# Optimization experiments

Measured on AMD Instinct MI355X. Metric: run time of the kernel, lower is better.

## Reference

```python
import jax, jax.numpy as jnp
import numpy as np

L = 50
N_INIT = 3.5      # initial radius n
N_STEP = 0.5      # n_step
NUM_ADJ_PARM = 0.1
NUM_CANDS = 256   # candidate radii n + k*n_step


def _leaky(x):
    return jax.nn.leaky_relu(x, negative_slope=0.01)


def _conv(x, w, b):
    y = jax.lax.conv_general_dilated(x, w, (1, 1), 'VALID',
                                     dimension_numbers=('NCHW', 'OIHW', 'NCHW'))
    return y + b[None, :, None, None]


def _maxpool2(x):
    return jax.lax.reduce_window(x, -jnp.inf, jax.lax.max,
                                 (1, 1, 2, 2), (1, 1, 2, 2), 'VALID')


def _sage(x, adj, w_rel, b_rel, w_root):
    # PyG DenseSAGEConv: lin_rel(mean-agg) + lin_root(x), normalize=False
    agg = adj @ x
    deg = jnp.clip(jnp.sum(adj, axis=-1, keepdims=True), 1.0, None)
    return (agg / deg) @ w_rel.T + b_rel + x @ w_root.T


def _build_adj(h):
    # fused pairwise euclidean distance + radius threshold with retry:
    # smallest radius in {n + k*n_step} whose (directed) edge count >= 0.1*N
    g = h @ h.T                                   # [N,N] gram
    sq = jnp.diag(g)
    dist = jnp.sqrt(jnp.maximum(sq[:, None] - 2.0 * g + sq[None, :], 0.0))
    n = h.shape[0]
    eye = jnp.eye(n, dtype=bool)
    d_sorted = jnp.sort(jnp.where(eye, jnp.inf, dist).reshape(-1))
    cands = N_INIT + N_STEP * jnp.arange(NUM_CANDS, dtype=dist.dtype)
    counts = jnp.searchsorted(d_sorted, cands)    # edges with dist < cand
    thr = cands[jnp.argmax(counts >= NUM_ADJ_PARM * n)]
    A = ((dist < thr) & (~eye)).astype(h.dtype)
    return jax.lax.stop_gradient(A)               # edge list is non-diff in torch too


def _diff_pool(z, a, s):
    # PyG dense_diff_pool (link + entropy losses; only link loss l1 is returned)
    s = jax.nn.softmax(s, axis=-1)
    x = s.T @ z
    adj = s.T @ a @ s
    l1 = jnp.linalg.norm(a - s @ s.T) / (a.shape[0] * a.shape[1])
    return x, adj, l1


def setup_inputs() -> dict:
    key = jax.random.key(0)
    ks = jax.random.split(key, 19)
    def w(k, shape, scale=0.05):
        return scale * jax.random.normal(k, shape, dtype=jnp.float32)
    N = 4096  # bag size / number of graph nodes
    return {
        'x': jax.random.normal(ks[0], (1, N, 1, 28, 28), dtype=jnp.float32),
        'conv1_w': w(ks[1], (20, 1, 5, 5)),
        'conv1_b': w(ks[2], (20,)),
        'conv2_w': w(ks[3], (50, 20, 5, 5)),
        'conv2_b': w(ks[4], (50,)),
        'fc_w': w(ks[5], (50, 800)),
        'fc_b': w(ks[6], (50,)),
        'embd_rel_w': w(ks[7], (50, 50)),
        'embd_rel_b': w(ks[8], (50,)),
        'embd_root_w': w(ks[9], (50, 50)),
        'pool_rel_w': w(ks[10], (1, 50)),
        'pool_rel_b': w(ks[11], (1,)),
        'pool_root_w': w(ks[12], (1, 50)),
        'mlp_w': w(ks[13], (1, 1)),
        'mlp_b': w(ks[14], (1,)),
        'lin1_w': w(ks[15], (25, 50)),
        'lin1_b': w(ks[16], (25,)),
        'lin2_w': w(ks[17], (2, 25)),
        'lin2_b': w(ks[18], (2,)),
    }


def reference(x, conv1_w, conv1_b, conv2_w, conv2_b, fc_w, fc_b,
              embd_rel_w, embd_rel_b, embd_root_w,
              pool_rel_w, pool_rel_b, pool_root_w,
              mlp_w, mlp_b, lin1_w, lin1_b, lin2_w, lin2_b):
    xi = x[0]                                             # squeeze(0): [N,1,28,28]
    h = _maxpool2(jax.nn.relu(_conv(xi, conv1_w, conv1_b)))   # [N,20,12,12]
    h = _maxpool2(jax.nn.relu(_conv(h, conv2_w, conv2_b)))    # [N,50,4,4]
    h = h.reshape(h.shape[0], -1)                         # [N,800]
    h = jax.nn.relu(h @ fc_w.T + fc_b)                    # [N,50]
    A = _build_adj(h)                                     # [N,N] dense adjacency
    Z = _leaky(_sage(h, A, embd_rel_w, embd_rel_b, embd_root_w))   # [N,50]
    S = _leaky(_sage(h, A, pool_rel_w, pool_rel_b, pool_root_w))   # [N,1]
    S = _leaky(S @ mlp_w.T + mlp_b)                       # [N,1]
    Xp, adjp, l1 = _diff_pool(Z, A, S)                    # [1,50], [1,1]
    Xp = _leaky(_sage(Xp, adjp, embd_rel_w, embd_rel_b, embd_root_w))  # reuses gnn_embd
    v = Xp.reshape(-1)                                    # [50]
    v = _leaky(v @ lin1_w.T + lin1_b)                     # [25]
    v = _leaky(v @ lin2_w.T + lin2_b)                     # [2]
    p = jax.nn.softmax(v, axis=0)
    return jnp.max(p), jnp.argmax(p), l1
```

## Files before the change

### kernel.cpp

```cpp
#include <hip/hip_runtime.h>
#include <hip/hip_bf16.h>

#define AGG_OFF     0u
#define DEG_OFF     819200u
#define XP_OFF      835584u
#define HIST_OFF    835840u
#define SCAL_OFF    836992u
#define S_OFF       837120u
#define H_OFF       1048576u
#define HT_OFF      1867776u
#define SQ_OFF      2686976u
#define BYTES_OFF   2703360u
#define WS_NEED     (2703360ull + 16777216ull)

__global__ __launch_bounds__(256) void mil_init(unsigned int* __restrict__ w)
{
    w[(size_t)blockIdx.x * 256u + threadIdx.x] = 0u;
}

__global__ __launch_bounds__(256, 2) void mil_cnn(
    const float* __restrict__ x, const float* __restrict__ w1, const float* __restrict__ b1,
    const float* __restrict__ w2, const float* __restrict__ b2,
    const float* __restrict__ fcw, const float* __restrict__ fcb,
    float* __restrict__ hout, float* __restrict__ hT, float* __restrict__ sqout)
{
    __shared__ __align__(16) float pool1[20*144];
    __shared__ __align__(16) float pool2[800];
    __shared__ float b1s[20];
    __shared__ float b2s[64];
    __shared__ float hloc[64];
    __shared__ __align__(16) float ovl[3200];

    float* img = ovl;
    float* w1s = ovl + 784;
    float* w2s = ovl;

    const int n = blockIdx.x;
    const int t = threadIdx.x;

    const float* xin = x + (size_t)n * 784;
    for (int i = t; i < 784; i += 256) img[i] = xin[i];
    for (int i = t; i < 500; i += 256) w1s[i] = w1[i];
    if (t < 20) b1s[t] = b1[t];
    { int u = t - 32; if (u >= 0 && u < 50) b2s[u] = b2[u]; }
    __syncthreads();

    if (t < 240) {
        const int c = t / 12, py = t % 12;
        float wr[25];
#pragma unroll
        for (int k = 0; k < 25; k++) wr[k] = w1s[c*25 + k];
        float acc0[24], acc1[24];
#pragma unroll
        for (int i = 0; i < 24; i++) { acc0[i] = 0.f; acc1[i] = 0.f; }
#pragma unroll
        for (int j = 0; j < 6; j++) {
            float rr[28];
            const float* rp = &img[(2*py + j)*28];
#pragma unroll
            for (int q = 0; q < 7; q++) {
                const float4 v = *(const float4*)(rp + 4*q);
                rr[4*q+0] = v.x; rr[4*q+1] = v.y; rr[4*q+2] = v.z; rr[4*q+3] = v.w;
            }
            if (j <= 4) {
#pragma unroll
                for (int kx = 0; kx < 5; kx++) {
                    const float wv = wr[j*5 + kx];
#pragma unroll
                    for (int xo = 0; xo < 24; xo++)
                        acc0[xo] = fmaf(rr[xo+kx], wv, acc0[xo]);
                }
            }
            if (j >= 1) {
#pragma unroll
                for (int kx = 0; kx < 5; kx++) {
                    const float wv = wr[(j-1)*5 + kx];
#pragma unroll
                    for (int xo = 0; xo < 24; xo++)
                        acc1[xo] = fmaf(rr[xo+kx], wv, acc1[xo]);
                }
            }
        }
        const float bias = b1s[c];
#pragma unroll
        for (int px = 0; px < 12; px++) {
            float v = fmaxf(fmaxf(acc0[2*px], acc0[2*px+1]),
                            fmaxf(acc1[2*px], acc1[2*px+1]));
            pool1[c*144 + py*12 + px] = fmaxf(v + bias, 0.f);
        }
    }
    __syncthreads();

    float acc2[16];
#pragma unroll
    for (int i = 0; i < 16; i++) acc2[i] = 0.f;
    const int c2 = t >> 2, py2 = t & 3;
    const int rswz = (c2 & 7) << 2;
    for (int cig = 0; cig < 10; cig++) {
        __syncthreads();
        for (int idx = t; idx < 3200; idx += 256) {
            const int cc = idx >> 6, cl = (idx >> 5) & 1, k = idx & 31;
            const float v = (k < 25) ? w2[cc*500 + (cig*2 + cl)*25 + k] : 0.f;
            w2s[(idx & ~31) | (k ^ ((cc & 7) << 2))] = v;
        }
        __syncthreads();
        if (t < 200) {
#pragma unroll
            for (int cl = 0; cl < 2; cl++) {
                const int ci = cig*2 + cl;
                float wreg[25];
                const int wbase = c2*64 + cl*32;
#pragma unroll
                for (int g = 0; g < 6; g++) {
                    const float4 v = *(const float4*)&w2s[wbase + (4*g ^ rswz)];
                    wreg[4*g+0] = v.x; wreg[4*g+1] = v.y;
                    wreg[4*g+2] = v.z; wreg[4*g+3] = v.w;
                }
                wreg[24] = w2s[wbase + (24 ^ rswz)];
#pragma unroll
                for (int j = 0; j < 6; j++) {
                    float rr[12];
                    const float* rp = &pool1[ci*144 + (2*py2 + j)*12];
#pragma unroll
                    for (int q = 0; q < 3; q++) {
                        const float4 v = *(const float4*)(rp + 4*q);
                        rr[4*q+0] = v.x; rr[4*q+1] = v.y;
                        rr[4*q+2] = v.z; rr[4*q+3] = v.w;
                    }
                    if (j <= 4) {
#pragma unroll
                        for (int kx = 0; kx < 5; kx++) {
                            const float wv = wreg[j*5 + kx];
#pragma unroll
                            for (int xo = 0; xo < 8; xo++)
                                acc2[xo] = fmaf(rr[xo+kx], wv, acc2[xo]);
                        }
                    }
                    if (j >= 1) {
#pragma unroll
                        for (int kx = 0; kx < 5; kx++) {
                            const float wv = wreg[(j-1)*5 + kx];
#pragma unroll
                            for (int xo = 0; xo < 8; xo++)
                                acc2[8+xo] = fmaf(rr[xo+kx], wv, acc2[8+xo]);
                        }
                    }
                }
            }
        }
    }
    __syncthreads();
    if (t < 200) {
        const float bias = b2s[c2];
#pragma unroll
        for (int px = 0; px < 4; px++) {
            float v = fmaxf(fmaxf(acc2[2*px], acc2[2*px+1]),
                            fmaxf(acc2[8+2*px], acc2[8+2*px+1]));
            pool2[c2*16 + py2*4 + px] = fmaxf(v + bias, 0.f);
        }
    }
    __syncthreads();

    {
        const int wv = t >> 6, lane = t & 63;
        for (int o = wv; o < 50; o += 4) {
            float acc = 0.f;
#pragma unroll
            for (int r = 0; r < 13; r++) {
                const int k = r*64 + lane;
                if (k < 800) acc = fmaf(fcw[o*800 + k], pool2[k], acc);
            }
#pragma unroll
            for (int off = 32; off > 0; off >>= 1) acc += __shfl_xor(acc, off);
            if (lane == 0) hloc[o] = fmaxf(acc + fcb[o], 0.f);
        }
    }
    __syncthreads();
    if (t < 50) {
        const float v = hloc[t];
        hout[(size_t)n*50 + t] = v;
        hT[(size_t)t*4096 + n] = v;
    }
    if (t < 64) {
        float s = (t < 50) ? hloc[t]*hloc[t] : 0.f;
#pragma unroll
        for (int off = 32; off > 0; off >>= 1) s += __shfl_xor(s, off);
        if (t == 0) sqout[n] = s;
    }
}

__global__ __launch_bounds__(256) void mil_colsum(
    const float* __restrict__ hT, float* __restrict__ S)
{
    __shared__ float red[4];
    const int d = blockIdx.x, t = threadIdx.x;
    float s = 0.f;
    for (int nn = t; nn < 4096; nn += 256) s += hT[(size_t)d*4096 + nn];
#pragma unroll
    for (int off = 32; off > 0; off >>= 1) s += __shfl_xor(s, off);
    if ((t & 63) == 0) red[t >> 6] = s;
    __syncthreads();
    if (t == 0) S[d] = red[0] + red[1] + red[2] + red[3];
}

__global__ __launch_bounds__(256, 3) void mil_hist(
    const float* __restrict__ hT, const float* __restrict__ sq,
    unsigned int* __restrict__ hist, unsigned char* __restrict__ bytesA,
    const int wb)
{
    __shared__ __align__(16) float hiT[6400];
    __shared__ __align__(16) float hjT[6400];
    __shared__ float sqi[128], sqj[128];
    __shared__ unsigned int lh[257];

    const int t = threadIdx.x;
    const int i0 = blockIdx.x * 128, j0 = blockIdx.y * 128;

    for (int idx = t; idx < 6400; idx += 256) {
        const int c = idx >> 7, l = idx & 127;
        hiT[idx] = hT[(size_t)c*4096 + i0 + l];
        hjT[idx] = hT[(size_t)c*4096 + j0 + l];
    }
    if (t < 128) { sqi[t] = sq[i0 + t]; sqj[t] = sq[j0 + t]; }
    for (int idx = t; idx < 257; idx += 256) lh[idx] = 0;
    __syncthreads();

    const int ti = t >> 4, tj = t & 15;
    float acc[8][8];
#pragma unroll
    for (int a = 0; a < 8; a++)
#pragma unroll
        for (int b = 0; b < 8; b++) acc[a][b] = 0.f;

    for (int c = 0; c < 50; c++) {
        const float4 a0 = *(const float4*)&hiT[c*128 + ti*8];
        const float4 a1 = *(const float4*)&hiT[c*128 + ti*8 + 4];
        const float4 b0 = *(const float4*)&hjT[c*128 + tj*8];
        const float4 b1 = *(const float4*)&hjT[c*128 + tj*8 + 4];
        const float aa[8] = {a0.x,a0.y,a0.z,a0.w,a1.x,a1.y,a1.z,a1.w};
        const float bb[8] = {b0.x,b0.y,b0.z,b0.w,b1.x,b1.y,b1.z,b1.w};
#pragma unroll
        for (int a = 0; a < 8; a++)
#pragma unroll
            for (int b = 0; b < 8; b++)
                acc[a][b] = fmaf(aa[a], bb[b], acc[a][b]);
    }

    unsigned int cnt0 = 0;
#pragma unroll
    for (int a = 0; a < 8; a++) {
        unsigned pk0 = 0, pk1 = 0;
#pragma unroll
        for (int b = 0; b < 8; b++) {
            const int gi = i0 + ti*8 + a, gj = j0 + tj*8 + b;
            int kbyte = 255;
            if (gi != gj) {
                const float d2 = sqi[ti*8+a] + sqj[tj*8+b] - 2.f*acc[a][b];
                const float d = sqrtf(fmaxf(d2, 0.f));
                int k = (int)floorf((d - 3.5f)*2.f) + 1;
                k = k < 0 ? 0 : (k > 256 ? 256 : k);
                if (k > 0   && d <  3.5f + 0.5f*(float)(k-1)) k--;
                if (k < 256 && d >= 3.5f + 0.5f*(float)k)     k++;
                if (k == 0) cnt0++;
                else atomicAdd(&lh[k], 1u);
                kbyte = k < 255 ? k : 255;
            }
            if (b < 4) pk0 |= (unsigned)kbyte << (8*b);
            else       pk1 |= (unsigned)kbyte << (8*(b-4));
        }
        if (wb) {
            const int gi = i0 + ti*8 + a;
            *(uint2*)&bytesA[(size_t)gi*4096 + j0 + tj*8] = make_uint2(pk0, pk1);
        }
    }
#pragma unroll
    for (int off = 32; off > 0; off >>= 1) cnt0 += __shfl_xor(cnt0, off);
    if ((t & 63) == 0 && cnt0) atomicAdd(&lh[0], cnt0);
    __syncthreads();
    for (int idx = t; idx < 257; idx += 256)
        if (lh[idx]) atomicAdd(&hist[idx], lh[idx]);
}

__global__ void mil_scan(const unsigned int* __restrict__ hist, int* __restrict__ scal)
{
    if (threadIdx.x == 0) {
        unsigned long long cum = 0, nz = 0;
        int kc = -1;
        for (int k = 0; k < 256; k++) {
            cum += hist[k];
            if (kc < 0 && cum >= 410ull) { kc = k; nz = cum; }
        }
        if (kc < 0) { kc = 0; nz = hist[0]; }
        scal[0] = kc;
        scal[1] = (int)nz;
        scal[2] = (nz * 2ull > 16773120ull) ? 1 : 0;
        scal[3] = (kc >= 255) ? 1 : 0;
    }
}

__global__ __launch_bounds__(256) void mil_agg_b(
    const float* __restrict__ h, const unsigned char* __restrict__ bytesA,
    const int* __restrict__ scal, float* __restrict__ agg, float* __restrict__ deg)
{
    __shared__ __align__(16) unsigned char bL[64*528];
    __shared__ __align__(16) float hsub[4096];
    if (scal[3] != 0) return;
    const int t = threadIdx.x;
    const int i0 = blockIdx.x * 64;
    const int jg = blockIdx.y * 512;
    const int kc = scal[0];
    const bool inv = (scal[2] != 0);

    for (int idx = t; idx < 2048; idx += 256) {
        const int r = idx >> 5, c = idx & 31;
        *(uint4*)&bL[r*528 + c*16] =
            *(const uint4*)&bytesA[(size_t)(i0 + r)*4096 + jg + c*16];
    }

    const int il = t >> 2, dq = t & 3;
    const int gi = i0 + il;
    float accum[16];
#pragma unroll
    for (int i = 0; i < 16; i++) accum[i] = 0.f;
    int degc = 0;

    for (int js = 0; js < 8; js++) {
        __syncthreads();
        for (int idx = t; idx < 4096; idx += 256) {
            const int jj = idx >> 6, d = idx & 63;
            hsub[idx] = (d < 50) ? h[(size_t)(jg + js*64 + jj)*50 + d] : 0.f;
        }
        __syncthreads();
        const unsigned char* brow = &bL[il*528 + js*64];
        const int jbase = jg + js*64;
        for (int jj = 0; jj < 64; jj++) {
            const bool e = (jbase + jj != gi) && ((brow[jj] <= kc) != inv);
            if (!__any(e)) continue;
            const float m = e ? 1.f : 0.f;
            if (e && dq == 0) degc++;
#pragma unroll
            for (int q = 0; q < 4; q++) {
                const float4 hv = *(const float4*)&hsub[jj*64 + dq*16 + q*4];
                accum[q*4+0] = fmaf(m, hv.x, accum[q*4+0]);
                accum[q*4+1] = fmaf(m, hv.y, accum[q*4+1]);
                accum[q*4+2] = fmaf(m, hv.z, accum[q*4+2]);
                accum[q*4+3] = fmaf(m, hv.w, accum[q*4+3]);
            }
        }
    }

#pragma unroll
    for (int q = 0; q < 4; q++)
#pragma unroll
        for (int rr = 0; rr < 4; rr++) {
            const int d = dq*16 + q*4 + rr;
            if (d < 50 && accum[q*4+rr] != 0.f)
                atomicAdd(&agg[(size_t)gi*50 + d], accum[q*4+rr]);
        }
    if (dq == 0 && degc) atomicAdd(&deg[gi], (float)degc);
}

__global__ __launch_bounds__(256, 3) void mil_agg_r(
    const float* __restrict__ h, const float* __restrict__ hT, const float* __restrict__ sq,
    const int* __restrict__ scal, float* __restrict__ agg, float* __restrict__ deg,
    const int mode)
{
    __shared__ __align__(16) float hiT[3200];
    __shared__ __align__(16) float hjT[3200];
    __shared__ float sqi[64], sqj[64];
    __shared__ __align__(16) float hsub[4096];
    __shared__ __align__(16) unsigned char mk[4096];

    if (mode == 1 && scal[3] == 0) return;
    const int t = threadIdx.x;
    const int i0 = blockIdx.x * 64;
    const float thr = 3.5f + 0.5f * (float)scal[0];
    const bool inv = (scal[2] != 0);

    for (int idx = t; idx < 3200; idx += 256) {
        const int c = idx >> 6, l = idx & 63;
        hiT[idx] = hT[(size_t)c*4096 + i0 + l];
    }
    if (t < 64) sqi[t] = sq[i0 + t];

    const int ti = t >> 4, tj = t & 15;
    const int il = t >> 2, dq = t & 3;
    float accum[16];
#pragma unroll
    for (int i = 0; i < 16; i++) accum[i] = 0.f;
    int degc = 0;

    for (int js = 0; js < 8; js++) {
        const int j0 = blockIdx.y * 512 + js * 64;
        __syncthreads();
        for (int idx = t; idx < 3200; idx += 256) {
            const int c = idx >> 6, l = idx & 63;
            hjT[idx] = hT[(size_t)c*4096 + j0 + l];
        }
        for (int idx = t; idx < 4096; idx += 256) {
            const int jj = idx >> 6, d = idx & 63;
            hsub[idx] = (d < 50) ? h[(size_t)(j0 + jj)*50 + d] : 0.f;
        }
        if (t < 64) sqj[t] = sq[j0 + t];
        __syncthreads();

        float acc[4][4];
#pragma unroll
        for (int a = 0; a < 4; a++)
#pragma unroll
            for (int b = 0; b < 4; b++) acc[a][b] = 0.f;
        for (int c = 0; c < 50; c++) {
            const float4 av = *(const float4*)&hiT[c*64 + ti*4];
            const float4 bv = *(const float4*)&hjT[c*64 + tj*4];
            const float aa[4] = {av.x, av.y, av.z, av.w};
            const float bb[4] = {bv.x, bv.y, bv.z, bv.w};
#pragma unroll
            for (int a = 0; a < 4; a++)
#pragma unroll
                for (int b = 0; b < 4; b++)
                    acc[a][b] = fmaf(aa[a], bb[b], acc[a][b]);
        }

#pragma unroll
        for (int b = 0; b < 4; b++) {
            unsigned char ob[4];
#pragma unroll
            for (int a = 0; a < 4; a++) {
                const int gi = i0 + ti*4 + a, gj = j0 + tj*4 + b;
                const float d2 = sqi[ti*4+a] + sqj[tj*4+b] - 2.f*acc[a][b];
                const float dd = sqrtf(fmaxf(d2, 0.f));
                const bool edge = (dd < thr);
                ob[a] = (gi != gj && (edge != inv)) ? 1 : 0;
            }
            *(uchar4*)&mk[(tj*4+b)*64 + ti*4] = make_uchar4(ob[0], ob[1], ob[2], ob[3]);
        }
        __syncthreads();

        for (int jj = 0; jj < 64; jj++) {
            const bool e = (mk[jj*64 + il] != 0);
            if (!__any(e)) continue;
            const float m = e ? 1.f : 0.f;
            if (e && dq == 0) degc++;
#pragma unroll
            for (int q = 0; q < 4; q++) {
                const float4 hv = *(const float4*)&hsub[jj*64 + dq*16 + q*4];
                accum[q*4+0] = fmaf(m, hv.x, accum[q*4+0]);
                accum[q*4+1] = fmaf(m, hv.y, accum[q*4+1]);
                accum[q*4+2] = fmaf(m, hv.z, accum[q*4+2]);
                accum[q*4+3] = fmaf(m, hv.w, accum[q*4+3]);
            }
        }
    }

    const int node = i0 + il;
#pragma unroll
    for (int q = 0; q < 4; q++)
#pragma unroll
        for (int rr = 0; rr < 4; rr++) {
            const int d = dq*16 + q*4 + rr;
            if (d < 50 && accum[q*4+rr] != 0.f)
                atomicAdd(&agg[(size_t)node*50 + d], accum[q*4+rr]);
        }
    if (dq == 0 && degc) atomicAdd(&deg[node], (float)degc);
}

__global__ __launch_bounds__(256) void mil_sage(
    const float* __restrict__ h, const float* __restrict__ agg, const float* __restrict__ deg,
    const float* __restrict__ S, const int* __restrict__ scal,
    const float* __restrict__ relw, const float* __restrict__ relb,
    const float* __restrict__ rootw, float* __restrict__ Xp)
{
    __shared__ float relT[2500];
    __shared__ float rootT[2500];
    __shared__ float rb[50];
    __shared__ float hn[250], mn[250], zb[250];
    const int t = threadIdx.x;
    const int nb = blockIdx.x * 5;
    const bool inv = (scal[2] != 0);

    for (int idx = t; idx < 2500; idx += 256) {
        const int d = idx / 50, c = idx % 50;
        relT[c*50 + d]  = relw[idx];
        rootT[c*50 + d] = rootw[idx];
    }
    if (t < 50) rb[t] = relb[t];
    if (t < 250) {
        const int nl = t / 50, d = t % 50;
        const int node = nb + nl;
        if (node < 4096) {
            const float hv = h[(size_t)node*50 + d];
            float av = agg[(size_t)node*50 + d];
            float dg = deg[node];
            if (inv) { av = S[d] - hv - av; dg = 4095.f - dg; }
            hn[t] = hv;
            mn[t] = av / fmaxf(dg, 1.f);
        } else { hn[t] = 0.f; mn[t] = 0.f; }
    }
    __syncthreads();
    if (t < 250) {
        const int nl = t / 50, d = t % 50;
        float z = rb[d];
        for (int c = 0; c < 50; c++) {
            z = fmaf(mn[nl*50 + c], relT[c*50 + d], z);
            z = fmaf(hn[nl*50 + c], rootT[c*50 + d], z);
        }
        z = z > 0.f ? z : 0.01f * z;
        zb[t] = (nb + nl < 4096) ? z : 0.f;
    }
    __syncthreads();
    if (t < 50) {
        float s = 0.f;
#pragma unroll
        for (int nl = 0; nl < 5; nl++) s += zb[nl*50 + t];
        atomicAdd(&Xp[t], s);
    }
}

__global__ void mil_final(
    const float* __restrict__ Xp, const int* __restrict__ scal,
    const float* __restrict__ relw, const float* __restrict__ relb,
    const float* __restrict__ rootw,
    const float* __restrict__ l1w, const float* __restrict__ l1b,
    const float* __restrict__ l2w, const float* __restrict__ l2b,
    float* __restrict__ out)
{
    __shared__ float xp[50], x2[50], v1[25], v2[2];
    const int t = threadIdx.x;
    if (t < 50) xp[t] = Xp[t];
    __syncthreads();
    const float adjp = (float)scal[1];
    const float dmax = fmaxf(adjp, 1.f);
    if (t < 50) {
        float z = relb[t];
        for (int c = 0; c < 50; c++) {
            const float mnc = (adjp * xp[c]) / dmax;
            z = fmaf(mnc,   relw[t*50 + c], z);
            z = fmaf(xp[c], rootw[t*50 + c], z);
        }
        x2[t] = z > 0.f ? z : 0.01f*z;
    }
    __syncthreads();
    if (t < 25) {
        float v = l1b[t];
        for (int c = 0; c < 50; c++) v = fmaf(l1w[t*50 + c], x2[c], v);
        v1[t] = v > 0.f ? v : 0.01f*v;
    }
    __syncthreads();
    if (t < 2) {
        float v = l2b[t];
        for (int c = 0; c < 25; c++) v = fmaf(l2w[t*25 + c], v1[c], v);
        v2[t] = v > 0.f ? v : 0.01f*v;
    }
    __syncthreads();
    if (t == 0) {
        const float a = v2[0], b = v2[1];
        const float mx = fmaxf(a, b);
        const float e0 = expf(a - mx), e1 = expf(b - mx);
        const float s = e0 + e1;
        const float p0 = e0 / s, p1 = e1 / s;
        const float pm = fmaxf(p0, p1);
        const float am = (p1 > p0) ? 1.f : 0.f;
        const int nnz = scal[1];
        const float l1v = sqrtf((float)(16777216 - nnz)) / 16777216.f;
        out[0] = pm;
        out[1] = am;
        out[2] = l1v;
    }
}

extern "C" void kernel_launch(void* const* d_in, const int* in_sizes, int n_in,
                              void* d_out, int out_size, void* d_ws, size_t ws_size,
                              hipStream_t stream)
{
    (void)in_sizes; (void)n_in; (void)out_size;
    const float* x     = (const float*)d_in[0];
    const float* w1    = (const float*)d_in[1];
    const float* b1    = (const float*)d_in[2];
    const float* w2    = (const float*)d_in[3];
    const float* b2    = (const float*)d_in[4];
    const float* fcw   = (const float*)d_in[5];
    const float* fcb   = (const float*)d_in[6];
    const float* relw  = (const float*)d_in[7];
    const float* relb  = (const float*)d_in[8];
    const float* rootw = (const float*)d_in[9];
    const float* l1w   = (const float*)d_in[15];
    const float* l1b   = (const float*)d_in[16];
    const float* l2w   = (const float*)d_in[17];
    const float* l2b   = (const float*)d_in[18];

    char* ws = (char*)d_ws;
    float* agg = (float*)(ws + AGG_OFF);
    float* deg = (float*)(ws + DEG_OFF);
    float* Xp  = (float*)(ws + XP_OFF);
    unsigned int* hist = (unsigned int*)(ws + HIST_OFF);
    int* scal  = (int*)(ws + SCAL_OFF);
    float* S   = (float*)(ws + S_OFF);
    float* h   = (float*)(ws + H_OFF);
    float* hT  = (float*)(ws + HT_OFF);
    float* sq  = (float*)(ws + SQ_OFF);
    unsigned char* bytesA = (unsigned char*)(ws + BYTES_OFF);

    const int have_bytes = (ws_size >= WS_NEED) ? 1 : 0;

    mil_init<<<818, 256, 0, stream>>>((unsigned int*)d_ws);
    mil_cnn<<<4096, 256, 0, stream>>>(x, w1, b1, w2, b2, fcw, fcb, h, hT, sq);
    mil_colsum<<<50, 256, 0, stream>>>(hT, S);
    mil_hist<<<dim3(32, 32), 256, 0, stream>>>(hT, sq, hist, bytesA, have_bytes);
    mil_scan<<<1, 64, 0, stream>>>(hist, scal);
    if (have_bytes) {
        mil_agg_b<<<dim3(64, 8), 256, 0, stream>>>(h, bytesA, scal, agg, deg);
        mil_agg_r<<<dim3(64, 8), 256, 0, stream>>>(h, hT, sq, scal, agg, deg, 1);
    } else {
        mil_agg_r<<<dim3(64, 8), 256, 0, stream>>>(h, hT, sq, scal, agg, deg, 0);
    }
    mil_sage<<<820, 256, 0, stream>>>(h, agg, deg, S, scal, relw, relb, rootw, Xp);
    mil_final<<<1, 64, 0, stream>>>(Xp, scal, relw, relb, rootw,
                                    l1w, l1b, l2w, l2b, (float*)d_out);
}
```

Baseline: 524.8 us.

## Read padded conv2 weights from global memory instead of staging through LDS

Adds a small pre-kernel that repacks the conv2 weights into a 28-float padded layout in the workspace. The conv2 loop then loads each thread's weights directly from global (L1/L2-cached) memory with float4 loads, which removes the 10 per-block shared-memory staging passes and their 20 block barriers. Shared memory use per block also drops, which may allow more resident blocks. The cost is an extra launch and global/cache weight loads inside the inner loop, which may stall more than LDS reads.

```diff
diff --git a/kernel.cpp b/kernel.cpp
--- a/kernel.cpp
+++ b/kernel.cpp
@@ -7,6 +7,7 @@
 #define HIST_OFF    835840u
 #define SCAL_OFF    836992u
 #define S_OFF       837120u
+#define W2P_OFF     839680u
 #define H_OFF       1048576u
 #define HT_OFF      1867776u
 #define SQ_OFF      2686976u
@@ -18,22 +19,29 @@
     w[(size_t)blockIdx.x * 256u + threadIdx.x] = 0u;
 }
 
+__global__ __launch_bounds__(256) void mil_wpad(
+    const float* __restrict__ w2, float* __restrict__ w2p)
+{
+    const int gid = blockIdx.x * 256 + threadIdx.x;
+    if (gid < 28000) {
+        const int k = gid % 28, rest = gid / 28;
+        w2p[gid] = (k < 25) ? w2[rest*25 + k] : 0.f;
+    }
+}
+
 __global__ __launch_bounds__(256, 2) void mil_cnn(
     const float* __restrict__ x, const float* __restrict__ w1, const float* __restrict__ b1,
-    const float* __restrict__ w2, const float* __restrict__ b2,
+    const float* __restrict__ w2p, const float* __restrict__ b2,
     const float* __restrict__ fcw, const float* __restrict__ fcb,
     float* __restrict__ hout, float* __restrict__ hT, float* __restrict__ sqout)
 {
     __shared__ __align__(16) float pool1[20*144];
     __shared__ __align__(16) float pool2[800];
+    __shared__ __align__(16) float img[784];
+    __shared__ float w1s[500];
     __shared__ float b1s[20];
     __shared__ float b2s[64];
     __shared__ float hloc[64];
-    __shared__ __align__(16) float ovl[3200];
-
-    float* img = ovl;
-    float* w1s = ovl + 784;
-    float* w2s = ovl;
 
     const int n = blockIdx.x;
     const int t = threadIdx.x;
@@ -95,62 +103,48 @@
 #pragma unroll
     for (int i = 0; i < 16; i++) acc2[i] = 0.f;
     const int c2 = t >> 2, py2 = t & 3;
-    const int rswz = (c2 & 7) << 2;
-    for (int cig = 0; cig < 10; cig++) {
-        __syncthreads();
-        for (int idx = t; idx < 3200; idx += 256) {
-            const int cc = idx >> 6, cl = (idx >> 5) & 1, k = idx & 31;
-            const float v = (k < 25) ? w2[cc*500 + (cig*2 + cl)*25 + k] : 0.f;
-            w2s[(idx & ~31) | (k ^ ((cc & 7) << 2))] = v;
-        }
-        __syncthreads();
-        if (t < 200) {
-#pragma unroll
-            for (int cl = 0; cl < 2; cl++) {
-                const int ci = cig*2 + cl;
-                float wreg[25];
-                const int wbase = c2*64 + cl*32;
-#pragma unroll
-                for (int g = 0; g < 6; g++) {
-                    const float4 v = *(const float4*)&w2s[wbase + (4*g ^ rswz)];
-                    wreg[4*g+0] = v.x; wreg[4*g+1] = v.y;
-                    wreg[4*g+2] = v.z; wreg[4*g+3] = v.w;
+    if (t < 200) {
+        const float* wch = w2p + c2*560;
+        for (int ci = 0; ci < 20; ci++) {
+            float wreg[25];
+            const float* wp = wch + ci*28;
+#pragma unroll
+            for (int g = 0; g < 6; g++) {
+                const float4 v = *(const float4*)(wp + 4*g);
+                wreg[4*g+0] = v.x; wreg[4*g+1] = v.y;
+                wreg[4*g+2] = v.z; wreg[4*g+3] = v.w;
+            }
+            wreg[24] = wp[24];
+#pragma unroll
+            for (int j = 0; j < 6; j++) {
+                float rr[12];
+                const float* rp = &pool1[ci*144 + (2*py2 + j)*12];
+#pragma unroll
+                for (int q = 0; q < 3; q++) {
+                    const float4 v = *(const float4*)(rp + 4*q);
+                    rr[4*q+0] = v.x; rr[4*q+1] = v.y;
+                    rr[4*q+2] = v.z; rr[4*q+3] = v.w;
                 }
-                wreg[24] = w2s[wbase + (24 ^ rswz)];
-#pragma unroll
-                for (int j = 0; j < 6; j++) {
-                    float rr[12];
-                    const float* rp = &pool1[ci*144 + (2*py2 + j)*12];
-#pragma unroll
-                    for (int q = 0; q < 3; q++) {
-                        const float4 v = *(const float4*)(rp + 4*q);
-                        rr[4*q+0] = v.x; rr[4*q+1] = v.y;
-                        rr[4*q+2] = v.z; rr[4*q+3] = v.w;
-                    }
-                    if (j <= 4) {
-#pragma unroll
-                        for (int kx = 0; kx < 5; kx++) {
-                            const float wv = wreg[j*5 + kx];
-#pragma unroll
-                            for (int xo = 0; xo < 8; xo++)
-                                acc2[xo] = fmaf(rr[xo+kx], wv, acc2[xo]);
-                        }
-                    }
-                    if (j >= 1) {
-#pragma unroll
-                        for (int kx = 0; kx < 5; kx++) {
-                            const float wv = wreg[(j-1)*5 + kx];
-#pragma unroll
-                            for (int xo = 0; xo < 8; xo++)
-                                acc2[8+xo] = fmaf(rr[xo+kx], wv, acc2[8+xo]);
-                        }
+                if (j <= 4) {
+#pragma unroll
+                    for (int kx = 0; kx < 5; kx++) {
+                        const float wv = wreg[j*5 + kx];
+#pragma unroll
+                        for (int xo = 0; xo < 8; xo++)
+                            acc2[xo] = fmaf(rr[xo+kx], wv, acc2[xo]);
                     }
                 }
-            }
-        }
-    }
-    __syncthreads();
-    if (t < 200) {
+                if (j >= 1) {
+#pragma unroll
+                    for (int kx = 0; kx < 5; kx++) {
+                        const float wv = wreg[(j-1)*5 + kx];
+#pragma unroll
+                        for (int xo = 0; xo < 8; xo++)
+                            acc2[8+xo] = fmaf(rr[xo+kx], wv, acc2[8+xo]);
+                    }
+                }
+            }
+        }
         const float bias = b2s[c2];
 #pragma unroll
         for (int px = 0; px < 4; px++) {
@@ -595,6 +589,7 @@
     unsigned int* hist = (unsigned int*)(ws + HIST_OFF);
     int* scal  = (int*)(ws + SCAL_OFF);
     float* S   = (float*)(ws + S_OFF);
+    float* w2p = (float*)(ws + W2P_OFF);
     float* h   = (float*)(ws + H_OFF);
     float* hT  = (float*)(ws + HT_OFF);
     float* sq  = (float*)(ws + SQ_OFF);
@@ -603,7 +598,8 @@
     const int have_bytes = (ws_size >= WS_NEED) ? 1 : 0;
 
     mil_init<<<818, 256, 0, stream>>>((unsigned int*)d_ws);
-    mil_cnn<<<4096, 256, 0, stream>>>(x, w1, b1, w2, b2, fcw, fcb, h, hT, sq);
+    mil_wpad<<<110, 256, 0, stream>>>(w2, w2p);
+    mil_cnn<<<4096, 256, 0, stream>>>(x, w1, b1, w2p, b2, fcw, fcb, h, hT, sq);
     mil_colsum<<<50, 256, 0, stream>>>(hT, S);
     mil_hist<<<dim3(32, 32), 256, 0, stream>>>(hT, sq, hist, bytesA, have_bytes);
     mil_scan<<<1, 64, 0, stream>>>(hist, scal);
```

After: 493.8 us. 1.06x faster.
